# Kernel tuning notes

Measured on AMD Instinct MI355X. Metric: run time of the kernel, lower is better.

The kernel has to match this reference:

```python
import jax, jax.numpy as jnp
import numpy as np

B, C, H, W = 8, 64, 96, 320
K = 50
HEAD = 256
CLS = 3
CIN3 = C + 2 + CLS  # feat + 2 coord maps + one-hot class


def _conv(x, w, b, pad):
    y = jax.lax.conv_general_dilated(x, w, (1, 1), [(pad, pad), (pad, pad)],
                                     dimension_numbers=('NCHW', 'OIHW', 'NCHW'))
    return y + b[None, :, None, None]


def _head2(x, w1, b1, w2, b2):
    # Conv3x3 -> ReLU -> Conv1x1 (heatmap / offset_2d / size_2d heads)
    return _conv(jax.nn.relu(_conv(x, w1, b1, 1)), w2, b2, 0)


def _head3(x, w1, b1, g, be, m, v, w2, b2):
    # Conv3x3 -> BN(eval) -> ReLU -> AdaptiveAvgPool2d(1) -> Conv1x1, returns [N, cout]
    y = _conv(x, w1, b1, 1)
    y = (y - m[None, :, None, None]) * (g * jax.lax.rsqrt(v + 1e-5))[None, :, None, None] + be[None, :, None, None]
    y = jax.nn.relu(y).mean((2, 3))
    return y @ w2.reshape(w2.shape[0], -1).T + b2


def _nms(heat):
    hmax = jax.lax.reduce_window(heat, -jnp.inf, jax.lax.max, (1, 1, 3, 3), (1, 1, 1, 1), 'SAME')
    return jnp.where(hmax == heat, heat, 0.0)


def _roi_align(feat, boxes, out=7, sr=2):
    # torchvision roi_align semantics (spatial_scale=1, aligned=False, sampling_ratio=2);
    # boxes are treated as constants w.r.t. gradients (as in torchvision).
    boxes = jax.lax.stop_gradient(boxes)
    b = boxes[:, 0].astype(jnp.int32)
    x1, y1, x2, y2 = boxes[:, 1], boxes[:, 2], boxes[:, 3], boxes[:, 4]
    bw = jnp.maximum(x2 - x1, 1.0) / out
    bh = jnp.maximum(y2 - y1, 1.0) / out
    g = (jnp.arange(out * sr, dtype=feat.dtype) + 0.5) / sr  # sample positions in bin units
    ys = y1[:, None] + g[None, :] * bh[:, None]  # [N, S]
    xs = x1[:, None] + g[None, :] * bw[:, None]
    Hf, Wf = feat.shape[2], feat.shape[3]
    def prep(c, dim):
        valid = (c >= -1.0) & (c <= dim)
        c = jnp.clip(c, 0.0, dim - 1.0)
        i0 = jnp.floor(c).astype(jnp.int32)
        i1 = jnp.minimum(i0 + 1, dim - 1)
        return i0, i1, c - i0, valid
    y0, y1i, fy, vy = prep(ys, Hf)
    x0, x1i, fx, vx = prep(xs, Wf)
    bb = b[:, None, None]
    def gather(yi, xi):
        return feat[bb, :, yi[:, :, None], xi[:, None, :]]  # [N, S, S, C]
    w00 = ((1 - fy)[:, :, None] * (1 - fx)[:, None, :])[..., None]
    w01 = ((1 - fy)[:, :, None] * fx[:, None, :])[..., None]
    w10 = (fy[:, :, None] * (1 - fx)[:, None, :])[..., None]
    w11 = (fy[:, :, None] * fx[:, None, :])[..., None]
    val = gather(y0, x0) * w00 + gather(y0, x1i) * w01 + gather(y1i, x0) * w10 + gather(y1i, x1i) * w11
    val = val * (vy[:, :, None] & vx[:, None, :])[..., None].astype(feat.dtype)
    N = boxes.shape[0]
    val = val.reshape(N, out, sr, out, sr, -1).mean((2, 4))  # avg over sampling grid
    return val.transpose(0, 3, 1, 2)  # [N, C, 7, 7]


def _project2rect(calib, p):
    f_u, f_v = calib[:, 0, 0], calib[:, 1, 1]
    c_u, c_v = calib[:, 0, 2], calib[:, 1, 2]
    b_x = calib[:, 0, 3] / -f_u
    b_y = calib[:, 1, 3] / -f_v
    x = (p[:, 0] - c_u) * p[:, 2] / f_u + b_x
    y = (p[:, 1] - c_v) * p[:, 2] / f_v + b_y
    return jnp.stack([x, y, p[:, 2]], -1)


def reference(feat, coord_ranges, calibs, mean_size, hm_w1, hm_b1, hm_w2, hm_b2, o2_w1, o2_b1, o2_w2, o2_b2, s2_w1, s2_b1, s2_w2, s2_b2, dep_w1, dep_b1, dep_g, dep_be, dep_m, dep_v, dep_w2, dep_b2, o3_w1, o3_b1, o3_g, o3_be, o3_m, o3_v, o3_w2, o3_b2, s3_w1, s3_b1, s3_g, s3_be, s3_m, s3_v, s3_w2, s3_b2, hd_w1, hd_b1, hd_g, hd_be, hd_m, hd_v, hd_w2, hd_b2):
    # dense 2D heads
    heatmap = _head2(feat, hm_w1, hm_b1, hm_w2, hm_b2)        # [B,1,H,W]
    offset_2d = _head2(feat, o2_w1, o2_b1, o2_w2, o2_b2)      # [B,2,H,W]
    size_2d = _head2(feat, s2_w1, s2_b1, s2_w2, s2_b2)        # [B,2,H,W]
    # test-mode: NMS + topK (single-class heatmap -> cls ids all 0)
    heat = _nms(jnp.clip(jax.nn.sigmoid(heatmap), 1e-4, 1.0 - 1e-4))
    _, inds = jax.lax.top_k(heat.reshape(B, -1), K)           # [B,K]
    cls_flat = jnp.zeros((B * K,), jnp.int32)
    # box2d maps in feature coords
    xg = jnp.arange(W, dtype=feat.dtype)
    yg = jnp.arange(H, dtype=feat.dtype)
    coord_map = jnp.stack([jnp.broadcast_to(xg[None, :], (H, W)), jnp.broadcast_to(yg[:, None], (H, W))], 0)
    centre = coord_map[None] + offset_2d
    box2d = jnp.concatenate([centre - size_2d / 2, centre + size_2d / 2], 1)  # [B,4,H,W]
    bidx = jnp.broadcast_to(jnp.arange(B, dtype=feat.dtype)[:, None, None, None], (B, 1, H, W))
    bm = jnp.concatenate([bidx, box2d], 1).reshape(B, 5, H * W)
    boxes = jnp.take_along_axis(bm, inds[:, None, :], 2).transpose(0, 2, 1).reshape(B * K, 5)
    roi = _roi_align(feat, boxes)                             # [N,64,7,7]
    bsel = boxes[:, 0].astype(jnp.int32)
    cr = coord_ranges[bsel]
    sx = cr[:, 1, 0] - cr[:, 0, 0]
    sy = cr[:, 1, 1] - cr[:, 0, 1]
    boxes_r = jnp.stack([boxes[:, 0],
                         boxes[:, 1] / W * sx + cr[:, 0, 0],
                         boxes[:, 2] / H * sy + cr[:, 0, 1],
                         boxes[:, 3] / W * sx + cr[:, 0, 0],
                         boxes[:, 4] / H * sy + cr[:, 0, 1]], -1)
    roi_calibs = calibs[bsel]
    ones = jnp.ones((B * K, 1), feat.dtype)
    p1 = _project2rect(roi_calibs, jnp.concatenate([boxes_r[:, 1:3], ones], -1))[:, :2]
    p2 = _project2rect(roi_calibs, jnp.concatenate([boxes_r[:, 3:5], ones], -1))[:, :2]
    cam = jnp.concatenate([p1, p2], -1)                       # [N,4]
    t = jnp.arange(7, dtype=feat.dtype) / 6.0
    xs7 = cam[:, 0:1] + t[None, :] * (cam[:, 2:3] - cam[:, 0:1])
    ys7 = cam[:, 1:2] + t[None, :] * (cam[:, 3:4] - cam[:, 1:2])
    cmx = jnp.broadcast_to(xs7[:, None, None, :], (B * K, 1, 7, 7))
    cmy = jnp.broadcast_to(ys7[:, None, :, None], (B * K, 1, 7, 7))
    hots = jax.nn.one_hot(cls_flat, CLS, dtype=feat.dtype)
    roi_full = jnp.concatenate([roi, cmx, cmy, jnp.broadcast_to(hots[:, :, None, None], (B * K, CLS, 7, 7))], 1)
    h2d = jnp.maximum(boxes_r[:, 4] - boxes_r[:, 2], 1.0)
    s3 = _head3(roi_full, s3_w1, s3_b1, s3_g, s3_be, s3_m, s3_v, s3_w2, s3_b2)  # [N,4]
    h3d_log_std = s3[:, 3:4]
    size3d_offset = s3[:, :3]
    size_3d = mean_size[cls_flat] + size3d_offset
    f_u = roi_calibs[:, 0, 0]
    depth_geo = size_3d[:, 0] / h2d * f_u
    dno = _head3(roi_full, dep_w1, dep_b1, dep_g, dep_be, dep_m, dep_v, dep_w2, dep_b2)  # [N,2]
    geo_log_std = (h3d_log_std[:, 0] + 2.0 * (jnp.log(f_u) - jnp.log(h2d)))[:, None]
    net_log_std = jax.nn.logsumexp(jnp.concatenate([dno[:, 1:2], geo_log_std], -1), -1, keepdims=True)
    depth = jnp.concatenate([1.0 / (jax.nn.sigmoid(dno[:, 0:1]) + 1e-6) - 1.0 + depth_geo[:, None], net_log_std], -1)
    heading = _head3(roi_full, hd_w1, hd_b1, hd_g, hd_be, hd_m, hd_v, hd_w2, hd_b2)
    offset_3d = _head3(roi_full, o3_w1, o3_b1, o3_g, o3_be, o3_m, o3_v, o3_w2, o3_b2)
    return (heatmap, offset_2d, size_2d, heading, depth, offset_3d, size3d_offset, h3d_log_std)


def setup_inputs() -> dict:
    keys = iter(jax.random.split(jax.random.key(0), 40))
    def rn(shape, s=0.05):
        return jax.random.normal(next(keys), shape, jnp.float32) * s
    d = {}
    d['feat'] = jax.random.normal(next(keys), (B, C, H, W), jnp.float32)
    d['coord_ranges'] = jnp.tile(jnp.array([[0.0, 0.0], [1280.0, 384.0]], jnp.float32)[None], (B, 1, 1))
    d['calibs'] = jnp.tile(jnp.array([[720.0, 0.0, 640.0, 0.04], [0.0, 720.0, 190.0, 0.01], [0.0, 0.0, 1.0, 0.003]], jnp.float32)[None], (B, 1, 1))
    d['mean_size'] = jnp.array([[1.52, 1.63, 3.88], [1.73, 0.67, 0.88], [1.77, 0.60, 1.76]], jnp.float32)
    for pfx, cout in [('hm', 1), ('o2', 2), ('s2', 2)]:
        d[pfx + '_w1'] = rn((HEAD, C, 3, 3))
        d[pfx + '_b1'] = jnp.zeros((HEAD,), jnp.float32)
        d[pfx + '_w2'] = rn((cout, HEAD, 1, 1))
        d[pfx + '_b2'] = jnp.full((cout,), -2.19, jnp.float32) if pfx == 'hm' else jnp.zeros((cout,), jnp.float32)
    for pfx, cout in [('dep', 2), ('o3', 2), ('s3', 4), ('hd', 24)]:
        d[pfx + '_w1'] = rn((HEAD, CIN3, 3, 3))
        d[pfx + '_b1'] = jnp.zeros((HEAD,), jnp.float32)
        d[pfx + '_g'] = jnp.ones((HEAD,), jnp.float32)
        d[pfx + '_be'] = jnp.zeros((HEAD,), jnp.float32)
        d[pfx + '_m'] = jnp.zeros((HEAD,), jnp.float32)
        d[pfx + '_v'] = jnp.ones((HEAD,), jnp.float32)
        d[pfx + '_w2'] = rn((cout, HEAD, 1, 1))
        d[pfx + '_b2'] = jnp.zeros((cout,), jnp.float32)
    return d
```

## Files before the change

kernel.cpp:

```cpp
#include <hip/hip_runtime.h>


constexpr int OFF_O2    = 245760;
constexpr int OFF_S2    = 737280;
constexpr int OFF_HEAD  = 1228800;
constexpr int OFF_DEPTH = 1238400;
constexpr int OFF_O3D   = 1239200;
constexpr int OFF_S3D   = 1240000;
constexpr int OFF_H3D   = 1241200;

constexpr int WS_W1T  = 0;
constexpr int WS_BNSC = 635904;
constexpr int WS_BNSH = 636928;
constexpr int WS_KEEP = 637952;
constexpr int WS_INDS = 883712;
constexpr int WS_BOX  = 884112;
constexpr int WS_XS7  = 885712;
constexpr int WS_YS7  = 888512;
constexpr int WS_FU   = 891312;
constexpr int WS_H2D  = 891712;
constexpr int WS_DNO  = 892112;
constexpr int WS_ROIF = 892912;
constexpr int WS_SIG  = WS_ROIF;
constexpr int WS_W1R  = 2245312;
constexpr int WS_WPACK2 = 2245312;
constexpr int WS_FEATH  = 2540224;
constexpr int WS_FEATL  = 10618560;
constexpr long long FAST_REQ_BYTES = 18696896LL * 4;
constexpr int WS_WPACK3 = 18696896;
constexpr int WS_A3     = 19139264;
constexpr long long FAST3_REQ_BYTES = 20694464LL * 4;

typedef __attribute__((ext_vector_type(4))) float f32x4;
typedef __attribute__((ext_vector_type(8))) _Float16 f16x8;
typedef __attribute__((ext_vector_type(4))) unsigned int u32x4;

__global__ void repack_kernel(
    const float* __restrict__ w2h, const float* __restrict__ w2o, const float* __restrict__ w2s,
    const float* __restrict__ w3d, const float* __restrict__ w3o, const float* __restrict__ w3s, const float* __restrict__ w3h,
    const float* __restrict__ g0, const float* __restrict__ be0, const float* __restrict__ m0, const float* __restrict__ v0,
    const float* __restrict__ g1, const float* __restrict__ be1, const float* __restrict__ m1, const float* __restrict__ v1,
    const float* __restrict__ g2, const float* __restrict__ be2, const float* __restrict__ m2, const float* __restrict__ v2,
    const float* __restrict__ g3, const float* __restrict__ be3, const float* __restrict__ m3, const float* __restrict__ v3,
    int skip2, int skip3, float* __restrict__ ws)
{
  int i = blockIdx.x * 256 + threadIdx.x;
  if (i < 3 * 147456) {
    if (skip2) return;
    int br = i / 147456, r = i - br * 147456, q = r >> 8, c = r & 255;
    const float* src = br == 0 ? w2h : (br == 1 ? w2o : w2s);
    ws[WS_W1R + i] = src[c * 576 + q];
  } else if (i < 3 * 147456 + 4 * 158976) {
    if (skip3) return;
    int j = i - 3 * 147456;
    int br = j / 158976, r = j - br * 158976, q = r >> 8, c = r & 255;
    const float* src = br == 0 ? w3d : (br == 1 ? w3o : (br == 2 ? w3s : w3h));
    ws[WS_W1T + j] = src[c * 621 + q];
  } else {
    int j = i - (3 * 147456 + 4 * 158976);
    if (j < 1024) {
      int br = j >> 8, c = j & 255;
      const float* g  = br == 0 ? g0  : (br == 1 ? g1  : (br == 2 ? g2  : g3));
      const float* be = br == 0 ? be0 : (br == 1 ? be1 : (br == 2 ? be2 : be3));
      const float* m  = br == 0 ? m0  : (br == 1 ? m1  : (br == 2 ? m2  : m3));
      const float* v  = br == 0 ? v0  : (br == 1 ? v1  : (br == 2 ? v2  : v3));
      float sc = g[c] * rsqrtf(v[c] + 1e-5f);
      ws[WS_BNSC + j] = sc;
      ws[WS_BNSH + j] = be[c] - m[c] * sc;
    }
  }
}

__global__ void wpack2_kernel(const float* __restrict__ hm_w1, const float* __restrict__ o2_w1,
                              const float* __restrict__ s2_w1, float* __restrict__ ws)
{
  int i = blockIdx.x * 256 + threadIdx.x;
  if (i >= 4 * 18 * 256 * 32) return;
  int br = i / 147456; int r = i - br * 147456;
  int c = r / 8192; int r2 = r - c * 8192;
  int n = r2 >> 5; int kk = r2 & 31;
  int kg = c * 32 + kk;
  int tap = kg >> 6, ci = kg & 63;
  const float* w1 = (br == 0) ? o2_w1 : (br == 1 ? s2_w1 : hm_w1);
  float v = w1[n * 576 + ci * 9 + tap];
  _Float16 hi = (_Float16)v;
  _Float16 valh;
  if (br == 3) valh = (_Float16)(v - (float)hi);
  else valh = hi;
  unsigned short bits = __builtin_bit_cast(unsigned short, valh);
  long long didx = (((((long long)br * 18 + c) * 16 + (n >> 4)) * 4 + (kk >> 3)) * 128) + (n & 15) * 8 + (kk & 7);
  unsigned short* dst = (unsigned short*)(ws + WS_WPACK2);
  dst[didx] = bits;
}

__global__ void wpack3_kernel(const float* __restrict__ w3d, const float* __restrict__ w3o,
                              const float* __restrict__ w3s, const float* __restrict__ w3h,
                              float* __restrict__ ws)
{
  int i = blockIdx.x * 256 + threadIdx.x;
  if (i >= 4 * 27 * 256 * 32) return;
  int br = i / 221184; int r = i - br * 221184;
  int s = r / 8192; int r2 = r - s * 8192;
  int n = r2 >> 5; int kk = r2 & 31;
  int tap = s / 3; int cc = s - tap * 3;
  int ch = cc * 32 + kk;
  const float* w1 = br == 0 ? w3d : (br == 1 ? w3o : (br == 2 ? w3s : w3h));
  float v = (ch < 69) ? w1[n * 621 + ch * 9 + tap] : 0.f;
  unsigned short bits = __builtin_bit_cast(unsigned short, (_Float16)v);
  long long didx = (((((long long)br * 27 + s) * 16 + (n >> 4)) * 4 + (kk >> 3)) * 128) + (n & 15) * 8 + (kk & 7);
  ((unsigned short*)(ws + WS_WPACK3))[didx] = bits;
}

__global__ void pad_zero_kernel(float* __restrict__ ws)
{
  int i = blockIdx.x * 256 + threadIdx.x;
  if (i >= 428032) return;
  int arr = i / 214016; int r = i - arr * 214016;
  int px = r >> 5, q = r & 31;
  int b = px / 836, pr = px - b * 836;
  int yy, xx;
  if (pr < 322) { yy = 0; xx = pr; }
  else if (pr < 644) { yy = 97; xx = pr - 322; }
  else { int t = pr - 644; yy = 1 + (t >> 1); xx = (t & 1) * 321; }
  unsigned int* dst = (unsigned int*)(ws + (arr ? WS_FEATL : WS_FEATH));
  dst[((b * 98 + yy) * 322 + xx) * 32 + q] = 0u;
}

__global__ __launch_bounds__(256) void transpose_kernel(const float* __restrict__ feat, float* __restrict__ ws)
{
  __shared__ unsigned short T2[2][64 * 65];
  int bx = blockIdx.x;
  int b = bx / 480; int r = bx % 480; int y = r / 5; int x0 = (r % 5) * 64;
  int tid = threadIdx.x;
  int lx = tid & 63, grp = tid >> 6;
  #pragma unroll
  for (int it = 0; it < 16; ++it) {
    int ci = it * 4 + grp;
    float v = feat[(((b * 64 + ci) * 96 + y) * 320) + x0 + lx];
    _Float16 h = (_Float16)v;
    _Float16 l = (_Float16)(v - (float)h);
    T2[0][lx * 65 + ci] = __builtin_bit_cast(unsigned short, h);
    T2[1][lx * 65 + ci] = __builtin_bit_cast(unsigned short, l);
  }
  __syncthreads();
  unsigned int* fH = (unsigned int*)(ws + WS_FEATH);
  unsigned int* fL = (unsigned int*)(ws + WS_FEATL);
  #pragma unroll
  for (int it = 0; it < 16; ++it) {
    int unit = it * 256 + tid;
    int arr = unit >> 11; int un = unit & 2047;
    int x = un >> 5, pr = un & 31;
    unsigned int lo = T2[arr][x * 65 + pr * 2];
    unsigned int hi = T2[arr][x * 65 + pr * 2 + 1];
    unsigned int val = lo | (hi << 16);
    unsigned int* dst = arr ? fL : fH;
    dst[((b * 98 + y + 1) * 322 + (x0 + x + 1)) * 32 + pr] = val;
  }
}

__device__ __forceinline__ int tile_off_sw(int row, int x, int j) {
  return ((row * 66 + x) * 8 + (j ^ (x & 7))) * 16;
}

__global__ __launch_bounds__(256, 2) void head2_os_kernel(
    const float* __restrict__ ws,
    const float* __restrict__ b1o, const float* __restrict__ b1s,
    const float* __restrict__ w2o, const float* __restrict__ w2s,
    const float* __restrict__ b2o, const float* __restrict__ b2s,
    float* __restrict__ out)
{
  __shared__ unsigned char tile[3 * 8 * 66 * 16];
  __shared__ float red[512];
  const int tid = threadIdx.x;
  const int l = tid & 63, w = tid >> 6;
  const int bx = blockIdx.x;
  const int b = bx / 480; int r = bx % 480;
  const int y = r / 5; const int x0 = (r % 5) * 64;
  const unsigned short* fH = (const unsigned short*)(ws + WS_FEATH) + (size_t)b * (98 * 322 * 64);
  const _Float16* wpk = (const _Float16*)(ws + WS_WPACK2);

  for (int t = 0; t < 7; ++t) {
    int u = t * 256 + tid;
    if (u < 1584) {
      int row = u / 528; int rem = u - row * 528;
      int x = rem >> 3, j0 = rem & 7;
      u32x4 v = *(const u32x4*)(fH + ((y + row) * 322 + (x0 + x)) * 64 + j0 * 8);
      *(u32x4*)(tile + ((row * 8 + j0) * 66 + x) * 16) = v;
    }
  }
  __syncthreads();

  const int l15 = l & 15, lg = l >> 4;
  const int aBase = (lg * 66 + l15) * 16;

  #pragma unroll 1
  for (int br = 0; br < 2; ++br) {
    f32x4 acc[4][4];
    #pragma unroll
    for (int i = 0; i < 4; ++i)
      #pragma unroll
      for (int j = 0; j < 4; ++j) acc[i][j] = (f32x4)(0.f);

    const _Float16* wB = wpk + (((long long)(br * 18) * 16 + w * 4) * 4 + lg) * 128 + l15 * 8;

    #pragma unroll
    for (int s = 0; s < 18; ++s) {
      const int tap = s >> 1, half = s & 1;
      const int ky = tap / 3, kx = tap - ky * 3;
      const int stepOff = ((ky * 8 + half * 4) * 66 + kx) * 16;
      f16x8 af[4], bf[4];
      #pragma unroll
      for (int pf = 0; pf < 4; ++pf)
        af[pf] = *(const f16x8*)(tile + aBase + pf * 256 + stepOff);
      #pragma unroll
      for (int nf = 0; nf < 4; ++nf)
        bf[nf] = *(const f16x8*)(wB + s * 8192 + nf * 512);
      #pragma unroll
      for (int pf = 0; pf < 4; ++pf)
        #pragma unroll
        for (int nf = 0; nf < 4; ++nf)
          acc[pf][nf] = __builtin_amdgcn_mfma_f32_16x16x32_f16(af[pf], bf[nf], acc[pf][nf], 0, 0, 0);
    }

    const float* b1 = br == 0 ? b1o : b1s;
    const float* w2 = br == 0 ? w2o : w2s;
    const float* b2 = br == 0 ? b2o : b2s;
    float b1v_[4], w2v[2][4];
    #pragma unroll
    for (int nf = 0; nf < 4; ++nf) {
      int n = w * 64 + nf * 16 + l15;
      b1v_[nf] = b1[n];
      w2v[0][nf] = w2[n];
      w2v[1][nf] = w2[256 + n];
    }
    __syncthreads();
    #pragma unroll
    for (int pf = 0; pf < 4; ++pf) {
      #pragma unroll
      for (int rr = 0; rr < 4; ++rr) {
        float s0 = 0.f, s1 = 0.f;
        #pragma unroll
        for (int nf = 0; nf < 4; ++nf) {
          float yv = acc[pf][nf][rr] + b1v_[nf];
          yv = yv > 0.f ? yv : 0.f;
          s0 = fmaf(w2v[0][nf], yv, s0);
          s1 = fmaf(w2v[1][nf], yv, s1);
        }
        #pragma unroll
        for (int m = 1; m < 16; m <<= 1) {
          s0 += __shfl_xor(s0, m);
          s1 += __shfl_xor(s1, m);
        }
        if (l15 == 0) {
          int p = pf * 16 + lg * 4 + rr;
          red[(w * 2 + 0) * 64 + p] = s0;
          red[(w * 2 + 1) * 64 + p] = s1;
        }
      }
    }
    __syncthreads();
    if (tid < 128) {
      int p = tid & 63, o = tid >> 6;
      float s = red[(0 * 2 + o) * 64 + p] + red[(1 * 2 + o) * 64 + p] +
                red[(2 * 2 + o) * 64 + p] + red[(3 * 2 + o) * 64 + p] + b2[o];
      int base = (br == 0) ? OFF_O2 : OFF_S2;
      out[base + ((b * 2 + o) * 96 + y) * 320 + x0 + p] = s;
    }
  }
}

__global__ __launch_bounds__(256, 2) void head2_hm_kernel(
    const float* __restrict__ ws,
    const float* __restrict__ b1h, const float* __restrict__ w2h, const float* __restrict__ b2h,
    float* __restrict__ out, float* __restrict__ sig)
{
  __shared__ unsigned short tiles[2][3 * 66 * 64];
  __shared__ float red[256];
  const int tid = threadIdx.x;
  const int l = tid & 63, w = tid >> 6;
  const int bx = blockIdx.x;
  const int b = bx / 480; int r = bx % 480;
  const int y = r / 5; const int x0 = (r % 5) * 64;
  const unsigned short* fH = (const unsigned short*)(ws + WS_FEATH) + (size_t)b * (98 * 322 * 64);
  const unsigned short* fL = (const unsigned short*)(ws + WS_FEATL) + (size_t)b * (98 * 322 * 64);
  const _Float16* wpk = (const _Float16*)(ws + WS_WPACK2);

  for (int t = 0; t < 13; ++t) {
    int u = t * 256 + tid;
    if (u < 3168) {
      int arr = u >= 1584; int uu = u - arr * 1584;
      int row = uu / 528; int rem = uu - row * 528;
      int x = rem >> 3, j0 = rem & 7;
      const unsigned short* src = arr ? fL : fH;
      u32x4 v = *(const u32x4*)(src + ((y + row) * 322 + (x0 + x)) * 64 + j0 * 8);
      *(u32x4*)((char*)&tiles[arr][0] + tile_off_sw(row, x, j0)) = v;
    }
  }
  __syncthreads();

  const int l15 = l & 15, lg = l >> 4;

  f32x4 acc[4][4];
  #pragma unroll
  for (int i = 0; i < 4; ++i)
    #pragma unroll
    for (int j = 0; j < 4; ++j) acc[i][j] = (f32x4)(0.f);

  f16x8 AH0[4], AL0[4], AH1[4], AL1[4];
  f16x8 BH0[4], BL0[4], BH1[4], BL1[4];

  auto ldA = [&](f16x8* ah, f16x8* al, int s) {
    int tap = s >> 1, half = s & 1;
    int ky = tap / 3, kx = tap - ky * 3;
    #pragma unroll
    for (int pf = 0; pf < 4; ++pf) {
      int p = pf * 16 + l15;
      int off = tile_off_sw(ky, p + kx, half * 4 + lg);
      ah[pf] = *(const f16x8*)((const char*)&tiles[0][0] + off);
      al[pf] = *(const f16x8*)((const char*)&tiles[1][0] + off);
    }
  };
  auto ldB = [&](f16x8* bh, f16x8* bl, int s) {
    #pragma unroll
    for (int nf = 0; nf < 4; ++nf) {
      bh[nf] = *(const f16x8*)(wpk + (((2LL * 18 + s) * 16 + (w * 4 + nf)) * 4 + lg) * 128 + l15 * 8);
      bl[nf] = *(const f16x8*)(wpk + (((3LL * 18 + s) * 16 + (w * 4 + nf)) * 4 + lg) * 128 + l15 * 8);
    }
  };
  auto mm3 = [&](f16x8* ah, f16x8* al, f16x8* bh, f16x8* bl) {
    #pragma unroll
    for (int pf = 0; pf < 4; ++pf)
      #pragma unroll
      for (int nf = 0; nf < 4; ++nf)
        acc[pf][nf] = __builtin_amdgcn_mfma_f32_16x16x32_f16(ah[pf], bh[nf], acc[pf][nf], 0, 0, 0);
    #pragma unroll
    for (int pf = 0; pf < 4; ++pf)
      #pragma unroll
      for (int nf = 0; nf < 4; ++nf)
        acc[pf][nf] = __builtin_amdgcn_mfma_f32_16x16x32_f16(ah[pf], bl[nf], acc[pf][nf], 0, 0, 0);
    #pragma unroll
    for (int pf = 0; pf < 4; ++pf)
      #pragma unroll
      for (int nf = 0; nf < 4; ++nf)
        acc[pf][nf] = __builtin_amdgcn_mfma_f32_16x16x32_f16(al[pf], bh[nf], acc[pf][nf], 0, 0, 0);
  };

  ldA(AH0, AL0, 0); ldB(BH0, BL0, 0);
  #pragma unroll 1
  for (int s2 = 0; s2 < 9; ++s2) {
    const int s = s2 * 2;
    ldA(AH1, AL1, s + 1); ldB(BH1, BL1, s + 1);
    mm3(AH0, AL0, BH0, BL0);
    if (s2 < 8) { ldA(AH0, AL0, s + 2); ldB(BH0, BL0, s + 2); }
    mm3(AH1, AL1, BH1, BL1);
  }

  float b1v_[4], w2v[4];
  #pragma unroll
  for (int nf = 0; nf < 4; ++nf) {
    int n = w * 64 + nf * 16 + l15;
    b1v_[nf] = b1h[n];
    w2v[nf] = w2h[n];
  }
  __syncthreads();
  #pragma unroll
  for (int pf = 0; pf < 4; ++pf) {
    #pragma unroll
    for (int rr = 0; rr < 4; ++rr) {
      float s0 = 0.f;
      #pragma unroll
      for (int nf = 0; nf < 4; ++nf) {
        float yv = acc[pf][nf][rr] + b1v_[nf];
        yv = yv > 0.f ? yv : 0.f;
        s0 = fmaf(w2v[nf], yv, s0);
      }
      #pragma unroll
      for (int m = 1; m < 16; m <<= 1) s0 += __shfl_xor(s0, m);
      if (l15 == 0) red[w * 64 + pf * 16 + lg * 4 + rr] = s0;
    }
  }
  __syncthreads();
  if (tid < 64) {
    float s = red[tid] + red[64 + tid] + red[128 + tid] + red[192 + tid] + b2h[0];
    int idx = (b * 96 + y) * 320 + x0 + tid;
    out[idx] = s;
    float sg = 1.f / (1.f + expf(-s));
    sg = fminf(fmaxf(sg, 1e-4f), 1.f - 1e-4f);
    sig[idx] = sg;
  }
}

__global__ __launch_bounds__(256) void head2_kernel(
    const float* __restrict__ feat, const float* __restrict__ ws,
    const float* __restrict__ b1h, const float* __restrict__ b1o, const float* __restrict__ b1s,
    const float* __restrict__ w2h, const float* __restrict__ w2o, const float* __restrict__ w2s,
    const float* __restrict__ b2h, const float* __restrict__ b2o, const float* __restrict__ b2s,
    float* __restrict__ out)
{
  __shared__ float xs[32 * 10 * 34];
  const int tid = threadIdx.x;
  const int tx = tid & 31, ty = tid >> 5;
  const int x0 = blockIdx.x * 32, y0 = blockIdx.y * 8, bz = blockIdx.z;
  const int px = x0 + tx, py = y0 + ty;
  const float* w1r = ws + WS_W1R;

  #pragma unroll 1
  for (int br = 0; br < 3; ++br) {
    const float* wr = w1r + br * 147456;
    const float* b1 = br == 0 ? b1h : (br == 1 ? b1o : b1s);
    const float* w2 = br == 0 ? w2h : (br == 1 ? w2o : w2s);
    const int cout = (br == 0) ? 1 : 2;
    float acc0 = 0.f, acc1 = 0.f;
    #pragma unroll 1
    for (int c0 = 0; c0 < 256; c0 += 64) {
      float part[64];
      #pragma unroll
      for (int j = 0; j < 64; ++j) part[j] = 0.f;
      #pragma unroll 1
      for (int cc = 0; cc < 2; ++cc) {
        for (int i = tid; i < 32 * 10 * 34; i += 256) {
          int ci = i / 340; int rr = i - ci * 340; int ry = rr / 34; int rx = rr - ry * 34;
          int gy = y0 + ry - 1, gx = x0 + rx - 1;
          float v = 0.f;
          if ((unsigned)gy < 96u && (unsigned)gx < 320u)
            v = feat[((bz * 64 + cc * 32 + ci) * 96 + gy) * 320 + gx];
          xs[i] = v;
        }
        __syncthreads();
        #pragma unroll 1
        for (int ci = 0; ci < 32; ++ci) {
          const float* wp = wr + ((cc * 32 + ci) * 9) * 256 + c0;
          const float* xb = &xs[ci * 340 + ty * 34 + tx];
          #pragma unroll
          for (int k = 0; k < 9; ++k) {
            float xv = xb[(k / 3) * 34 + (k % 3)];
            const float* wk = wp + k * 256;
            #pragma unroll
            for (int j = 0; j < 64; ++j) part[j] = fmaf(wk[j], xv, part[j]);
          }
        }
        __syncthreads();
      }
      #pragma unroll
      for (int j = 0; j < 64; ++j) {
        float yv = part[j] + b1[c0 + j];
        yv = yv > 0.f ? yv : 0.f;
        acc0 = fmaf(w2[c0 + j], yv, acc0);
        if (cout > 1) acc1 = fmaf(w2[256 + c0 + j], yv, acc1);
      }
    }
    if (br == 0) {
      out[(bz * 96 + py) * 320 + px] = acc0 + b2h[0];
    } else if (br == 1) {
      out[OFF_O2 + ((bz * 2 + 0) * 96 + py) * 320 + px] = acc0 + b2o[0];
      out[OFF_O2 + ((bz * 2 + 1) * 96 + py) * 320 + px] = acc1 + b2o[1];
    } else {
      out[OFF_S2 + ((bz * 2 + 0) * 96 + py) * 320 + px] = acc0 + b2s[0];
      out[OFF_S2 + ((bz * 2 + 1) * 96 + py) * 320 + px] = acc1 + b2s[1];
    }
  }
}

__global__ void nms_sig_kernel(const float* __restrict__ out, float* __restrict__ sig)
{
  int i = blockIdx.x * 256 + threadIdx.x;
  if (i >= 8 * 30720) return;
  float s = 1.f / (1.f + expf(-out[i]));
  s = s < 1e-4f ? 1e-4f : s;
  float hi = 1.f - 1e-4f;
  sig[i] = s > hi ? hi : s;
}

__global__ void nms_max_kernel(const float* __restrict__ sig, float* __restrict__ keep)
{
  int i = blockIdx.x * 256 + threadIdx.x;
  if (i >= 8 * 30720) return;
  int b = i / 30720; int r = i - b * 30720; int y = r / 320; int x = r - y * 320;
  const float* sb = sig + b * 30720;
  float v = sb[y * 320 + x];
  float m = v;
  for (int dy = -1; dy <= 1; ++dy)
    for (int dx = -1; dx <= 1; ++dx) {
      int yy = y + dy, xx = x + dx;
      if (yy >= 0 && yy < 96 && xx >= 0 && xx < 320) m = fmaxf(m, sb[yy * 320 + xx]);
    }
  keep[i] = (m == v) ? v : 0.f;
}

__global__ __launch_bounds__(256) void topk_kernel(float* ws)
{
  constexpr int CAP = 6144;
  __shared__ float cv[CAP];
  __shared__ int   cix[CAP];
  __shared__ int   cnt;
  __shared__ float wv_[4];
  __shared__ int   wi_[4];
  __shared__ int   wsl[4];
  int b = blockIdx.x, tid = threadIdx.x;
  int lane = tid & 63, wid = tid >> 6;
  if (tid == 0) cnt = 0;
  __syncthreads();
  const float* kb = ws + WS_KEEP + b * 30720;
  for (int i = tid; i < 30720; i += 256) {
    float v = kb[i];
    if (v > 0.f) {
      int pos = atomicAdd(&cnt, 1);
      if (pos < CAP) { cv[pos] = v; cix[pos] = i; }
    }
  }
  __syncthreads();
  int ncand = cnt < CAP ? cnt : CAP;
  int* inds = (int*)(ws + WS_INDS);
  for (int k = 0; k < 50; ++k) {
    float bv = -1.f; int bi = 0x7fffffff; int bs = -1;
    for (int i = tid; i < ncand; i += 256) {
      float v = cv[i]; int id = cix[i];
      if (v > bv || (v == bv && id < bi)) { bv = v; bi = id; bs = i; }
    }
    #pragma unroll
    for (int m = 1; m < 64; m <<= 1) {
      float ov = __shfl_xor(bv, m);
      int oi = __shfl_xor(bi, m);
      int os_ = __shfl_xor(bs, m);
      if (ov > bv || (ov == bv && oi < bi)) { bv = ov; bi = oi; bs = os_; }
    }
    if (lane == 0) { wv_[wid] = bv; wi_[wid] = bi; wsl[wid] = bs; }
    __syncthreads();
    if (tid == 0) {
      float fv = wv_[0]; int fi = wi_[0]; int fs = wsl[0];
      #pragma unroll
      for (int t = 1; t < 4; ++t) {
        if (wv_[t] > fv || (wv_[t] == fv && wi_[t] < fi)) { fv = wv_[t]; fi = wi_[t]; fs = wsl[t]; }
      }
      inds[b * 50 + k] = fi;
      if (fs >= 0) cv[fs] = -1.f;
    }
    __syncthreads();
  }
}

__global__ void boxes_kernel(const float* __restrict__ out, const float* __restrict__ coord_ranges,
                             const float* __restrict__ calibs, float* ws)
{
  int n = blockIdx.x * 256 + threadIdx.x;
  if (n >= 400) return;
  const int* inds = (const int*)(ws + WS_INDS);
  int b = n / 50;
  int idx = inds[n];
  int iy = idx / 320, ix = idx - iy * 320;
  float o2x = out[OFF_O2 + ((b * 2 + 0) * 96 + iy) * 320 + ix];
  float o2y = out[OFF_O2 + ((b * 2 + 1) * 96 + iy) * 320 + ix];
  float sw  = out[OFF_S2 + ((b * 2 + 0) * 96 + iy) * 320 + ix];
  float sh  = out[OFF_S2 + ((b * 2 + 1) * 96 + iy) * 320 + ix];
  float cx = (float)ix + o2x, cy = (float)iy + o2y;
  float x1 = cx - sw * 0.5f, y1 = cy - sh * 0.5f, x2 = cx + sw * 0.5f, y2 = cy + sh * 0.5f;
  ws[WS_BOX + n * 4 + 0] = x1; ws[WS_BOX + n * 4 + 1] = y1;
  ws[WS_BOX + n * 4 + 2] = x2; ws[WS_BOX + n * 4 + 3] = y2;
  float cr00 = coord_ranges[b * 4 + 0], cr01 = coord_ranges[b * 4 + 1];
  float sx = coord_ranges[b * 4 + 2] - cr00, sy = coord_ranges[b * 4 + 3] - cr01;
  float x1r = x1 / 320.f * sx + cr00, y1r = y1 / 96.f * sy + cr01;
  float x2r = x2 / 320.f * sx + cr00, y2r = y2 / 96.f * sy + cr01;
  const float* cl = calibs + b * 12;
  float fu = cl[0], cu = cl[2], bx = cl[3] / (-fu);
  float fv = cl[5], cvv = cl[6], by = cl[7] / (-fv);
  float p1x = (x1r - cu) / fu + bx, p1y = (y1r - cvv) / fv + by;
  float p2x = (x2r - cu) / fu + bx, p2y = (y2r - cvv) / fv + by;
  #pragma unroll
  for (int j = 0; j < 7; ++j) {
    float t = (float)j / 6.f;
    ws[WS_XS7 + n * 7 + j] = p1x + t * (p2x - p1x);
    ws[WS_YS7 + n * 7 + j] = p1y + t * (p2y - p1y);
  }
  ws[WS_FU + n] = fu;
  ws[WS_H2D + n] = fmaxf(y2r - y1r, 1.f);
}

__global__ __launch_bounds__(256) void roi_kernel(const float* __restrict__ feat, int fast3, float* ws)
{
  int n = blockIdx.x;
  int tid = threadIdx.x;
  __shared__ int   iy0[14], iy1[14], ix0[14], ix1[14];
  __shared__ float fy[14], fx[14], vy[14], vx[14];
  float bx1 = ws[WS_BOX + n * 4], by1 = ws[WS_BOX + n * 4 + 1];
  float bx2 = ws[WS_BOX + n * 4 + 2], by2 = ws[WS_BOX + n * 4 + 3];
  if (tid < 14) {
    float bh = fmaxf(by2 - by1, 1.f) / 7.f;
    float g = ((float)tid + 0.5f) * 0.5f;
    float c = by1 + g * bh;
    vy[tid] = (c >= -1.f && c <= 96.f) ? 1.f : 0.f;
    c = fminf(fmaxf(c, 0.f), 95.f);
    int i0 = (int)floorf(c);
    iy0[tid] = i0; iy1[tid] = (i0 + 1 < 95) ? i0 + 1 : 95;
    fy[tid] = c - (float)i0;
  } else if (tid < 28) {
    int t = tid - 14;
    float bw = fmaxf(bx2 - bx1, 1.f) / 7.f;
    float g = ((float)t + 0.5f) * 0.5f;
    float c = bx1 + g * bw;
    vx[t] = (c >= -1.f && c <= 320.f) ? 1.f : 0.f;
    c = fminf(fmaxf(c, 0.f), 319.f);
    int i0 = (int)floorf(c);
    ix0[t] = i0; ix1[t] = (i0 + 1 < 319) ? i0 + 1 : 319;
    fx[t] = c - (float)i0;
  }
  __syncthreads();
  int bsel = n / 50;
  const float* fbase = feat + bsel * 64 * 30720;
  float* rf = ws + WS_ROIF + n * 3381;
  for (int i = tid; i < 64 * 49; i += 256) {
    int c = i / 49, p = i - c * 49;
    int oy = p / 7, ox = p - oy * 7;
    const float* fb = fbase + c * 30720;
    float s = 0.f;
    #pragma unroll
    for (int sy2 = 0; sy2 < 2; ++sy2) {
      #pragma unroll
      for (int sx2 = 0; sx2 < 2; ++sx2) {
        int jy = oy * 2 + sy2, jx = ox * 2 + sx2;
        const float* r0 = fb + iy0[jy] * 320;
        const float* r1 = fb + iy1[jy] * 320;
        float gy = fy[jy], gx = fx[jx];
        float v00 = r0[ix0[jx]], v01 = r0[ix1[jx]], v10 = r1[ix0[jx]], v11 = r1[ix1[jx]];
        float v = v00 * (1.f - gy) * (1.f - gx) + v01 * (1.f - gy) * gx
                + v10 * gy * (1.f - gx) + v11 * gy * gx;
        s += v * vy[jy] * vx[jx];
      }
    }
    rf[c * 49 + p] = s * 0.25f;
  }
  if (tid < 5 * 49) {
    int ch = tid / 49, p = tid - ch * 49;
    int oy = p / 7, ox = p - oy * 7;
    float v;
    if (ch == 0) v = ws[WS_XS7 + n * 7 + ox];
    else if (ch == 1) v = ws[WS_YS7 + n * 7 + oy];
    else if (ch == 2) v = 1.f;
    else v = 0.f;
    rf[(64 + ch) * 49 + p] = v;
  }
  if (fast3) {
    __syncthreads();
    unsigned short* a3 = (unsigned short*)(ws + WS_A3) + (size_t)n * 7776;
    for (int t = 0; t < 31; ++t) {
      int i = t * 256 + tid;
      if (i < 7776) {
        int pr = i / 96, ch = i - pr * 96;
        int py = pr / 9, px = pr - py * 9;
        float v = 0.f;
        if (py >= 1 && py <= 7 && px >= 1 && px <= 7 && ch < 69)
          v = rf[ch * 49 + (py - 1) * 7 + (px - 1)];
        a3[i] = __builtin_bit_cast(unsigned short, (_Float16)v);
      }
    }
  }
}

__global__ __launch_bounds__(256, 2) void head3m_kernel(
    float* __restrict__ ws,
    const float* __restrict__ b1d, const float* __restrict__ b1o3, const float* __restrict__ b1s3, const float* __restrict__ b1hd,
    const float* __restrict__ w2d, const float* __restrict__ w2o3, const float* __restrict__ w2s3, const float* __restrict__ w2hd,
    const float* __restrict__ b2d, const float* __restrict__ b2o3, const float* __restrict__ b2s3, const float* __restrict__ b2hd,
    float* __restrict__ out)
{
  __shared__ unsigned char A[81 * 104 * 2];
  __shared__ float ym[256];
  const int tid = threadIdx.x;
  const int l = tid & 63, w = tid >> 6;
  const int l15 = l & 15, lg = l >> 4;
  const int n = blockIdx.x;
  const unsigned short* a3 = (const unsigned short*)(ws + WS_A3) + (size_t)n * 7776;
  const _Float16* wp3 = (const _Float16*)(ws + WS_WPACK3);

  #pragma unroll
  for (int t = 0; t < 4; ++t) {
    int u = t * 256 + tid;
    if (u < 972) {
      int row = u / 12, cu = u - row * 12;
      u32x4 v = *(const u32x4*)(a3 + u * 8);
      *(u32x4*)(A + (row * 104 + cu * 8) * 2) = v;
    }
  }
  __syncthreads();

  int aB[4];
  #pragma unroll
  for (int pf = 0; pf < 4; ++pf) {
    int p = pf * 16 + l15;
    int rb = (p < 49) ? ((p / 7) * 9 + (p % 7)) : 0;
    aB[pf] = rb * 208 + lg * 16;
  }

  #pragma unroll 1
  for (int br = 0; br < 4; ++br) {
    const float* b1 = br == 0 ? b1d : (br == 1 ? b1o3 : (br == 2 ? b1s3 : b1hd));
    const float* w2 = br == 0 ? w2d : (br == 1 ? w2o3 : (br == 2 ? w2s3 : w2hd));
    const float* b2 = br == 0 ? b2d : (br == 1 ? b2o3 : (br == 2 ? b2s3 : b2hd));
    const int cout = br == 0 ? 2 : (br == 1 ? 2 : (br == 2 ? 4 : 24));

    f32x4 acc[4][4];
    #pragma unroll
    for (int i = 0; i < 4; ++i)
      #pragma unroll
      for (int j = 0; j < 4; ++j) acc[i][j] = (f32x4)(0.f);

    const _Float16* wB3 = wp3 + (((long long)(br * 27) * 16 + w * 4) * 4 + lg) * 128 + l15 * 8;

    #pragma unroll
    for (int s = 0; s < 27; ++s) {
      const int tap = s / 3, cc = s - tap * 3;
      const int ky = tap / 3, kx = tap - ky * 3;
      const int stepOff = (ky * 9 + kx) * 208 + cc * 64;
      f16x8 af[4], bf[4];
      #pragma unroll
      for (int pf = 0; pf < 4; ++pf)
        af[pf] = *(const f16x8*)(A + aB[pf] + stepOff);
      #pragma unroll
      for (int nf = 0; nf < 4; ++nf)
        bf[nf] = *(const f16x8*)(wB3 + s * 8192 + nf * 512);
      #pragma unroll
      for (int pf = 0; pf < 4; ++pf)
        #pragma unroll
        for (int nf = 0; nf < 4; ++nf)
          acc[pf][nf] = __builtin_amdgcn_mfma_f32_16x16x32_f16(af[pf], bf[nf], acc[pf][nf], 0, 0, 0);
    }

    #pragma unroll
    for (int nf = 0; nf < 4; ++nf) {
      int nn = w * 64 + nf * 16 + l15;
      float b1n = b1[nn];
      float scn = ws[WS_BNSC + br * 256 + nn];
      float shn = ws[WS_BNSH + br * 256 + nn];
      float local = 0.f;
      #pragma unroll
      for (int pf = 0; pf < 4; ++pf) {
        #pragma unroll
        for (int rr = 0; rr < 4; ++rr) {
          int p = pf * 16 + lg * 4 + rr;
          float yv = (acc[pf][nf][rr] + b1n) * scn + shn;
          yv = yv > 0.f ? yv : 0.f;
          local += (p < 49) ? yv : 0.f;
        }
      }
      local += __shfl_xor(local, 16);
      local += __shfl_xor(local, 32);
      if (lg == 0) ym[nn] = local;
    }
    __syncthreads();
    for (int o = w; o < cout; o += 4) {
      float p = 0.f;
      #pragma unroll
      for (int t = 0; t < 4; ++t) p = fmaf(w2[o * 256 + t * 64 + l], ym[t * 64 + l], p);
      p *= (1.f / 49.f);
      #pragma unroll
      for (int off = 32; off > 0; off >>= 1) p += __shfl_down(p, off);
      if (l == 0) {
        float v = p + b2[o];
        if (br == 0) ws[WS_DNO + n * 2 + o] = v;
        else if (br == 1) out[OFF_O3D + n * 2 + o] = v;
        else if (br == 2) { if (o < 3) out[OFF_S3D + n * 3 + o] = v; else out[OFF_H3D + n] = v; }
        else out[OFF_HEAD + n * 24 + o] = v;
      }
    }
    __syncthreads();
  }
}

__global__ __launch_bounds__(256) void head3_kernel(
    float* ws,
    const float* __restrict__ b1d, const float* __restrict__ b1o3, const float* __restrict__ b1s3, const float* __restrict__ b1hd,
    const float* __restrict__ w2d, const float* __restrict__ w2o3, const float* __restrict__ w2s3, const float* __restrict__ w2hd,
    const float* __restrict__ b2d, const float* __restrict__ b2o3, const float* __restrict__ b2s3, const float* __restrict__ b2hd,
    float* __restrict__ out)
{
  int n = blockIdx.x, br = blockIdx.y;
  int c = threadIdx.x;
  __shared__ float ym[256];
  const float* wt = ws + WS_W1T + br * 158976;
  const float* b1 = br == 0 ? b1d : (br == 1 ? b1o3 : (br == 2 ? b1s3 : b1hd));
  const float* w2 = br == 0 ? w2d : (br == 1 ? w2o3 : (br == 2 ? w2s3 : w2hd));
  const float* b2 = br == 0 ? b2d : (br == 1 ? b2o3 : (br == 2 ? b2s3 : b2hd));
  const int cout = br == 0 ? 2 : (br == 1 ? 2 : (br == 2 ? 4 : 24));
  const float* xin0 = ws + WS_ROIF + n * 3381;

  float acc[49];
  #pragma unroll
  for (int i = 0; i < 49; ++i) acc[i] = 0.f;

  #pragma unroll 1
  for (int ci = 0; ci < 69; ++ci) {
    float wv[9];
    #pragma unroll
    for (int k = 0; k < 9; ++k) wv[k] = wt[(ci * 9 + k) * 256 + c];
    const float* xin = xin0 + ci * 49;
    #pragma unroll
    for (int y = 0; y < 7; ++y) {
      float xr[9];
      xr[0] = 0.f; xr[8] = 0.f;
      #pragma unroll
      for (int q = 0; q < 7; ++q) xr[q + 1] = xin[y * 7 + q];
      #pragma unroll
      for (int ky = 0; ky < 3; ++ky) {
        int pyy = y + 1 - ky;
        if (pyy >= 0 && pyy < 7) {
          #pragma unroll
          for (int kx = 0; kx < 3; ++kx) {
            float w = wv[ky * 3 + kx];
            #pragma unroll
            for (int pxx = 0; pxx < 7; ++pxx)
              acc[pyy * 7 + pxx] = fmaf(w, xr[pxx + kx], acc[pyy * 7 + pxx]);
          }
        }
      }
    }
  }
  float b1c = b1[c];
  float sc = ws[WS_BNSC + br * 256 + c];
  float sh = ws[WS_BNSH + br * 256 + c];
  float sum = 0.f;
  #pragma unroll
  for (int i = 0; i < 49; ++i) {
    float yv = (acc[i] + b1c) * sc + sh;
    sum += yv > 0.f ? yv : 0.f;
  }
  ym[c] = sum / 49.f;
  __syncthreads();
  int lane = c & 63, wid = c >> 6;
  for (int o = wid; o < cout; o += 4) {
    float p = 0.f;
    #pragma unroll
    for (int t = 0; t < 4; ++t) p = fmaf(w2[o * 256 + t * 64 + lane], ym[t * 64 + lane], p);
    #pragma unroll
    for (int off = 32; off > 0; off >>= 1) p += __shfl_down(p, off);
    if (lane == 0) {
      float v = p + b2[o];
      if (br == 0) ws[WS_DNO + n * 2 + o] = v;
      else if (br == 1) out[OFF_O3D + n * 2 + o] = v;
      else if (br == 2) { if (o < 3) out[OFF_S3D + n * 3 + o] = v; else out[OFF_H3D + n] = v; }
      else out[OFF_HEAD + n * 24 + o] = v;
    }
  }
}

__global__ void depth_kernel(const float* ws, const float* __restrict__ mean_size, float* __restrict__ out)
{
  int n = blockIdx.x * 256 + threadIdx.x;
  if (n >= 400) return;
  float h3d = out[OFF_H3D + n];
  float s30 = out[OFF_S3D + n * 3];
  float size0 = mean_size[0] + s30;
  float f = ws[WS_FU + n], h = ws[WS_H2D + n];
  float dgeo = size0 / h * f;
  float geo = h3d + 2.f * (logf(f) - logf(h));
  float a = ws[WS_DNO + n * 2 + 1];
  float mx = fmaxf(a, geo);
  float nls = mx + logf(expf(a - mx) + expf(geo - mx));
  float sg = 1.f / (1.f + expf(-ws[WS_DNO + n * 2]));
  out[OFF_DEPTH + n * 2] = 1.f / (sg + 1e-6f) - 1.f + dgeo;
  out[OFF_DEPTH + n * 2 + 1] = nls;
}

extern "C" void kernel_launch(void* const* d_in, const int* in_sizes, int n_in,
                              void* d_out, int out_size, void* d_ws, size_t ws_size,
                              hipStream_t stream)
{
  const float* feat         = (const float*)d_in[0];
  const float* coord_ranges = (const float*)d_in[1];
  const float* calibs       = (const float*)d_in[2];
  const float* mean_size    = (const float*)d_in[3];
  const float* hm_w1 = (const float*)d_in[4];
  const float* hm_b1 = (const float*)d_in[5];
  const float* hm_w2 = (const float*)d_in[6];
  const float* hm_b2 = (const float*)d_in[7];
  const float* o2_w1 = (const float*)d_in[8];
  const float* o2_b1 = (const float*)d_in[9];
  const float* o2_w2 = (const float*)d_in[10];
  const float* o2_b2 = (const float*)d_in[11];
  const float* s2_w1 = (const float*)d_in[12];
  const float* s2_b1 = (const float*)d_in[13];
  const float* s2_w2 = (const float*)d_in[14];
  const float* s2_b2 = (const float*)d_in[15];
  const float* dep_w1 = (const float*)d_in[16];
  const float* dep_b1 = (const float*)d_in[17];
  const float* dep_g  = (const float*)d_in[18];
  const float* dep_be = (const float*)d_in[19];
  const float* dep_m  = (const float*)d_in[20];
  const float* dep_v  = (const float*)d_in[21];
  const float* dep_w2 = (const float*)d_in[22];
  const float* dep_b2 = (const float*)d_in[23];
  const float* o3_w1 = (const float*)d_in[24];
  const float* o3_b1 = (const float*)d_in[25];
  const float* o3_g  = (const float*)d_in[26];
  const float* o3_be = (const float*)d_in[27];
  const float* o3_m  = (const float*)d_in[28];
  const float* o3_v  = (const float*)d_in[29];
  const float* o3_w2 = (const float*)d_in[30];
  const float* o3_b2 = (const float*)d_in[31];
  const float* s3_w1 = (const float*)d_in[32];
  const float* s3_b1 = (const float*)d_in[33];
  const float* s3_g  = (const float*)d_in[34];
  const float* s3_be = (const float*)d_in[35];
  const float* s3_m  = (const float*)d_in[36];
  const float* s3_v  = (const float*)d_in[37];
  const float* s3_w2 = (const float*)d_in[38];
  const float* s3_b2 = (const float*)d_in[39];
  const float* hd_w1 = (const float*)d_in[40];
  const float* hd_b1 = (const float*)d_in[41];
  const float* hd_g  = (const float*)d_in[42];
  const float* hd_be = (const float*)d_in[43];
  const float* hd_m  = (const float*)d_in[44];
  const float* hd_v  = (const float*)d_in[45];
  const float* hd_w2 = (const float*)d_in[46];
  const float* hd_b2 = (const float*)d_in[47];

  float* out = (float*)d_out;
  float* ws  = (float*)d_ws;
  bool fast  = (long long)ws_size >= FAST_REQ_BYTES;
  bool fast3 = (long long)ws_size >= FAST3_REQ_BYTES;

  repack_kernel<<<dim3((3 * 147456 + 4 * 158976 + 1024 + 255) / 256), 256, 0, stream>>>(
      hm_w1, o2_w1, s2_w1, dep_w1, o3_w1, s3_w1, hd_w1,
      dep_g, dep_be, dep_m, dep_v, o3_g, o3_be, o3_m, o3_v,
      s3_g, s3_be, s3_m, s3_v, hd_g, hd_be, hd_m, hd_v,
      fast ? 1 : 0, fast3 ? 1 : 0, ws);

  if (fast) {
    wpack2_kernel<<<dim3((4 * 18 * 256 * 32 + 255) / 256), 256, 0, stream>>>(hm_w1, o2_w1, s2_w1, ws);
    pad_zero_kernel<<<dim3((428032 + 255) / 256), 256, 0, stream>>>(ws);
    transpose_kernel<<<dim3(3840), 256, 0, stream>>>(feat, ws);
    head2_os_kernel<<<dim3(3840), 256, 0, stream>>>(ws, o2_b1, s2_b1, o2_w2, s2_w2, o2_b2, s2_b2, out);
    head2_hm_kernel<<<dim3(3840), 256, 0, stream>>>(ws, hm_b1, hm_w2, hm_b2, out, ws + WS_SIG);
  } else {
    head2_kernel<<<dim3(10, 12, 8), 256, 0, stream>>>(feat, ws,
        hm_b1, o2_b1, s2_b1, hm_w2, o2_w2, s2_w2, hm_b2, o2_b2, s2_b2, out);
    nms_sig_kernel<<<dim3(960), 256, 0, stream>>>(out, ws + WS_SIG);
  }
  if (fast3)
    wpack3_kernel<<<dim3((4 * 27 * 256 * 32 + 255) / 256), 256, 0, stream>>>(dep_w1, o3_w1, s3_w1, hd_w1, ws);

  nms_max_kernel<<<dim3(960), 256, 0, stream>>>(ws + WS_SIG, ws + WS_KEEP);
  topk_kernel<<<dim3(8), 256, 0, stream>>>(ws);
  boxes_kernel<<<dim3(2), 256, 0, stream>>>(out, coord_ranges, calibs, ws);
  roi_kernel<<<dim3(400), 256, 0, stream>>>(feat, fast3 ? 1 : 0, ws);
  if (fast3) {
    head3m_kernel<<<dim3(400), 256, 0, stream>>>(ws,
        dep_b1, o3_b1, s3_b1, hd_b1, dep_w2, o3_w2, s3_w2, hd_w2,
        dep_b2, o3_b2, s3_b2, hd_b2, out);
  } else {
    head3_kernel<<<dim3(400, 4), 256, 0, stream>>>(ws,
        dep_b1, o3_b1, s3_b1, hd_b1, dep_w2, o3_w2, s3_w2, hd_w2,
        dep_b2, o3_b2, s3_b2, hd_b2, out);
  }
  depth_kernel<<<dim3(2), 256, 0, stream>>>(ws, mean_size, out);
}
```

Before: 585.9 us.

## Use channel-group-major LDS layout and fully unroll heatmap head MMA loop

The heatmap head kernel's LDS tile changes from an XOR-swizzled pixel-major layout to a layout where each 8-channel group is stored contiguously across x positions. This makes A-fragment addresses a constant base plus compile-time step offsets. The manual double-buffered software pipeline (unroll 1, ping-pong registers) is replaced by a fully unrolled 18-step loop, so the compiler does the scheduling. The trade-off is more code size and register pressure, and the new layout may cause LDS bank conflicts, since lanes in a 16-group now read addresses 16 bytes apart across a 66-stride row.

```diff
diff --git a/kernel.cpp b/kernel.cpp
--- a/kernel.cpp
+++ b/kernel.cpp
@@ -158,9 +158,6 @@
   }
 }
 
-__device__ __forceinline__ int tile_off_sw(int row, int x, int j) {
-  return ((row * 66 + x) * 8 + (j ^ (x & 7))) * 16;
-}
 
 __global__ __launch_bounds__(256, 2) void head2_os_kernel(
     const float* __restrict__ ws,
@@ -274,7 +271,7 @@
     const float* __restrict__ b1h, const float* __restrict__ w2h, const float* __restrict__ b2h,
     float* __restrict__ out, float* __restrict__ sig)
 {
-  __shared__ unsigned short tiles[2][3 * 66 * 64];
+  __shared__ unsigned char tiles[2 * 3 * 8 * 66 * 16];
   __shared__ float red[256];
   const int tid = threadIdx.x;
   const int l = tid & 63, w = tid >> 6;
@@ -293,12 +290,13 @@
       int x = rem >> 3, j0 = rem & 7;
       const unsigned short* src = arr ? fL : fH;
       u32x4 v = *(const u32x4*)(src + ((y + row) * 322 + (x0 + x)) * 64 + j0 * 8);
-      *(u32x4*)((char*)&tiles[arr][0] + tile_off_sw(row, x, j0)) = v;
+      *(u32x4*)(tiles + arr * 25344 + ((row * 8 + j0) * 66 + x) * 16) = v;
     }
   }
   __syncthreads();
 
   const int l15 = l & 15, lg = l >> 4;
+  const int aBase = (lg * 66 + l15) * 16;
 
   f32x4 acc[4][4];
   #pragma unroll
@@ -306,28 +304,25 @@
     #pragma unroll
     for (int j = 0; j < 4; ++j) acc[i][j] = (f32x4)(0.f);
 
-  f16x8 AH0[4], AL0[4], AH1[4], AL1[4];
-  f16x8 BH0[4], BL0[4], BH1[4], BL1[4];
-
-  auto ldA = [&](f16x8* ah, f16x8* al, int s) {
-    int tap = s >> 1, half = s & 1;
-    int ky = tap / 3, kx = tap - ky * 3;
+  const _Float16* wBH = wpk + (((long long)(2 * 18) * 16 + w * 4) * 4 + lg) * 128 + l15 * 8;
+  const _Float16* wBL = wpk + (((long long)(3 * 18) * 16 + w * 4) * 4 + lg) * 128 + l15 * 8;
+
+  #pragma unroll
+  for (int s = 0; s < 18; ++s) {
+    const int tap = s >> 1, half = s & 1;
+    const int ky = tap / 3, kx = tap - ky * 3;
+    const int stepOff = ((ky * 8 + half * 4) * 66 + kx) * 16;
+    f16x8 ah[4], al[4], bh[4], bl[4];
     #pragma unroll
     for (int pf = 0; pf < 4; ++pf) {
-      int p = pf * 16 + l15;
-      int off = tile_off_sw(ky, p + kx, half * 4 + lg);
-      ah[pf] = *(const f16x8*)((const char*)&tiles[0][0] + off);
-      al[pf] = *(const f16x8*)((const char*)&tiles[1][0] + off);
-    }
-  };
-  auto ldB = [&](f16x8* bh, f16x8* bl, int s) {
+      ah[pf] = *(const f16x8*)(tiles + aBase + pf * 256 + stepOff);
+      al[pf] = *(const f16x8*)(tiles + 25344 + aBase + pf * 256 + stepOff);
+    }
     #pragma unroll
     for (int nf = 0; nf < 4; ++nf) {
-      bh[nf] = *(const f16x8*)(wpk + (((2LL * 18 + s) * 16 + (w * 4 + nf)) * 4 + lg) * 128 + l15 * 8);
-      bl[nf] = *(const f16x8*)(wpk + (((3LL * 18 + s) * 16 + (w * 4 + nf)) * 4 + lg) * 128 + l15 * 8);
-    }
-  };
-  auto mm3 = [&](f16x8* ah, f16x8* al, f16x8* bh, f16x8* bl) {
+      bh[nf] = *(const f16x8*)(wBH + s * 8192 + nf * 512);
+      bl[nf] = *(const f16x8*)(wBL + s * 8192 + nf * 512);
+    }
     #pragma unroll
     for (int pf = 0; pf < 4; ++pf)
       #pragma unroll
@@ -343,16 +338,6 @@
       #pragma unroll
       for (int nf = 0; nf < 4; ++nf)
         acc[pf][nf] = __builtin_amdgcn_mfma_f32_16x16x32_f16(al[pf], bh[nf], acc[pf][nf], 0, 0, 0);
-  };
-
-  ldA(AH0, AL0, 0); ldB(BH0, BL0, 0);
-  #pragma unroll 1
-  for (int s2 = 0; s2 < 9; ++s2) {
-    const int s = s2 * 2;
-    ldA(AH1, AL1, s + 1); ldB(BH1, BL1, s + 1);
-    mm3(AH0, AL0, BH0, BL0);
-    if (s2 < 8) { ldA(AH0, AL0, s + 2); ldB(BH0, BL0, s + 2); }
-    mm3(AH1, AL1, BH1, BL1);
   }
 
   float b1v_[4], w2v[4];
```

Measured after the change: 576.6 us. About the same (-1.6%).
